# Optimization experiments

Hardware: AMD Instinct MI355X
Metric: run time of the kernel (lower is better)

The kernel has to match this reference:

```python
import jax, jax.numpy as jnp
import numpy as np
import math

NUM_HEADS = 8


def _dwconv(x, w, b, pad):
    # depthwise conv: x (B,C,H,W), w (C,1,k,k)
    c = x.shape[1]
    y = jax.lax.conv_general_dilated(
        x, w, window_strides=(1, 1), padding=[(pad, pad), (pad, pad)],
        feature_group_count=c, dimension_numbers=("NCHW", "OIHW", "NCHW"))
    return y + b[None, :, None, None]


def _conv(x, w, b, pad):
    y = jax.lax.conv_general_dilated(
        x, w, window_strides=(1, 1), padding=[(pad, pad), (pad, pad)],
        dimension_numbers=("NCHW", "OIHW", "NCHW"))
    return y + b[None, :, None, None]


def setup_inputs() -> dict:
    key = jax.random.key(0)
    ks = jax.random.split(key, 6)
    B, C, H, W = 8, 128, 128, 128
    x = jax.random.normal(ks[0], (B, C, H, W), dtype=jnp.float32)
    wq = jax.random.normal(ks[1], (C, 1, 9, 9), dtype=jnp.float32) * 0.05
    wk = jax.random.normal(ks[2], (C, 1, 9, 9), dtype=jnp.float32) * 0.05
    wv = jax.random.normal(ks[3], (C, 1, 9, 9), dtype=jnp.float32) * 0.05
    wo = jax.random.normal(ks[4], (C, C, 3, 3), dtype=jnp.float32) * 0.02
    bq = jnp.zeros((C,), jnp.float32)
    bk = jnp.zeros((C,), jnp.float32)
    bv = jnp.zeros((C,), jnp.float32)
    bo = jnp.zeros((C,), jnp.float32)
    return {"x": x, "wq": wq, "bq": bq, "wk": wk, "bk": bk,
            "wv": wv, "bv": bv, "wo": wo, "bo": bo}


def reference(x, wq, bq, wk, bk, wv, bv, wo, bo):
    b, c, h, w = x.shape
    hds = NUM_HEADS
    d = (h * w) // hds  # spatial dim split across heads
    q = _dwconv(x, wq, bq, 4).reshape(b, c, hds, d).transpose(0, 2, 1, 3)  # (b,hds,c,d)
    k = _dwconv(x, wk, bk, 4).reshape(b, c, hds, d).transpose(0, 2, 3, 1)  # (b,hds,d,c)
    v = _dwconv(x, wv, bv, 4).reshape(b, c, hds, d).transpose(0, 2, 1, 3)  # (b,hds,c,d)
    # channel attention: C x C scores per head, fp32 softmax
    qk = jnp.einsum("bhcd,bhde->bhce", q.astype(jnp.float32), k.astype(jnp.float32)) / math.sqrt(h * w)
    a = jnp.einsum("bhce,bhed->bhcd", jax.nn.softmax(qk, axis=-1), v.astype(jnp.float32))
    a = a.transpose(0, 2, 1, 3).reshape(b, c, h, w)
    return _conv(a, wo, bo, 1)
```

## Files before the change

### kernel.cpp

```cpp
#include <hip/hip_runtime.h>

#define BATCH 8
#define CH 128
#define HH 128
#define WW 128
#define HWSZ 16384
#define NHEADS 8
#define DHEAD 2048

typedef short bf16x8 __attribute__((ext_vector_type(8)));
typedef short bf16x4v __attribute__((ext_vector_type(4)));
typedef float f32x4 __attribute__((ext_vector_type(4)));
typedef float f32x2 __attribute__((ext_vector_type(2)));
typedef _Float16 f16x8 __attribute__((ext_vector_type(8)));
typedef _Float16 f16x4 __attribute__((ext_vector_type(4)));

static __device__ inline unsigned short f2bf(float f) {
    unsigned u = __builtin_bit_cast(unsigned, f);
    u += 0x7fff + ((u >> 16) & 1);
    return (unsigned short)(u >> 16);
}

__global__ __launch_bounds__(256) void toeplitz_prep_kernel(
    const float* __restrict__ wq, const float* __restrict__ wk,
    const float* __restrict__ wv, _Float16* __restrict__ Tp)
{
    const int g = blockIdx.x * 256 + threadIdx.x;
    const int c    = g / 1728;
    const int rem  = g - c * 1728;
    const int m    = rem >> 6;
    const int lane = rem & 63;
    const int conv = m / 9;
    const int dy   = m - conv * 9;
    const float* w = (conv == 0) ? wq : ((conv == 1) ? wk : wv);
    const int j    = lane & 15;
    const int kb   = (lane >> 4) << 3;
    f16x8 h;
    #pragma unroll
    for (int e = 0; e < 8; ++e) {
        const int d = kb + e - j;
        h[e] = (d >= 0 && d <= 8) ? (_Float16)w[c * 81 + dy * 9 + d]
                                  : (_Float16)0.f;
    }
    *(f16x8*)&Tp[(size_t)g * 8] = h;
}

__global__ __launch_bounds__(256) void dwconv_qkv_mfma_kernel(
    const float* __restrict__ x,
    const float* __restrict__ bq, const float* __restrict__ bk,
    const float* __restrict__ bv,
    const _Float16* __restrict__ Tp,
    unsigned short* __restrict__ Qb, unsigned short* __restrict__ Kb,
    unsigned short* __restrict__ Vb)
{
    const int bc = blockIdx.x;
    const int b  = bc >> 7;
    const int c  = bc & (CH - 1);

    __shared__ _Float16 img[136][144];

    const int tid  = threadIdx.x;
    const int wave = tid >> 6;
    const int lane = tid & 63;
    const int lx   = lane & 15;
    const int qd   = lane >> 4;

    f16x8 Btp[27];
    const _Float16* tp = Tp + (size_t)c * 13824 + (size_t)lane * 8;
    #pragma unroll
    for (int m = 0; m < 27; ++m)
        Btp[m] = *(const f16x8*)(tp + (size_t)m * 512);

    {
        f16x8 z = {0, 0, 0, 0, 0, 0, 0, 0};
        _Float16* flat = &img[0][0];
        for (int i = tid; i < 2448; i += 256)
            *(f16x8*)&flat[i * 8] = z;
    }
    __syncthreads();
    const float* xp = x + (size_t)bc * HWSZ;
    for (int i = tid; i < 4096; i += 256) {
        const float4 v = *(const float4*)&xp[i * 4];
        const int y  = i >> 5;
        const int xc = (i & 31) << 2;
        f16x4 h = {(_Float16)v.x, (_Float16)v.y, (_Float16)v.z, (_Float16)v.w};
        *(f16x4*)&img[y + 4][xc + 4] = h;
    }
    __syncthreads();

    const float bqv = bq[c], bkv = bk[c], bvv = bv[c];

    #pragma unroll 1
    for (int t = 0; t < 8; ++t) {
        const int sg = t * 4 + wave;
        const int yg = sg >> 2;
        const int y0 = yg << 4;
        const int x0 = (sg & 3) << 5;

        f32x4 aq0 = {bqv, bqv, bqv, bqv}, aq1 = aq0;
        f32x4 ak0 = {bkv, bkv, bkv, bkv}, ak1 = ak0;
        f32x4 av0 = {bvv, bvv, bvv, bvv}, av1 = av0;

        const _Float16* rp = &img[y0 + lx][x0 + (qd << 3)];
        #pragma unroll
        for (int dy = 0; dy < 9; ++dy) {
            const f16x8 a0 = *(const f16x8*)rp;
            const f16x8 a1 = *(const f16x8*)(rp + 16);
            rp += 144;
            aq0 = __builtin_amdgcn_mfma_f32_16x16x32_f16(a0, Btp[dy],      aq0, 0, 0, 0);
            aq1 = __builtin_amdgcn_mfma_f32_16x16x32_f16(a1, Btp[dy],      aq1, 0, 0, 0);
            ak0 = __builtin_amdgcn_mfma_f32_16x16x32_f16(a0, Btp[9 + dy],  ak0, 0, 0, 0);
            ak1 = __builtin_amdgcn_mfma_f32_16x16x32_f16(a1, Btp[9 + dy],  ak1, 0, 0, 0);
            av0 = __builtin_amdgcn_mfma_f32_16x16x32_f16(a0, Btp[18 + dy], av0, 0, 0, 0);
            av1 = __builtin_amdgcn_mfma_f32_16x16x32_f16(a1, Btp[18 + dy], av1, 0, 0, 0);
        }

        const size_t base = ((size_t)(b * 8 + yg) * CH + c) * DHEAD
                          + (size_t)(qd << 2) * WW + x0 + lx;
        #pragma unroll
        for (int r = 0; r < 4; ++r) {
            Qb[base + r * WW]      = f2bf(aq0[r]);
            Qb[base + r * WW + 16] = f2bf(aq1[r]);
            Kb[base + r * WW]      = f2bf(ak0[r]);
            Kb[base + r * WW + 16] = f2bf(ak1[r]);
            Vb[base + r * WW]      = f2bf(av0[r]);
            Vb[base + r * WW + 16] = f2bf(av1[r]);
        }
    }
}

__global__ __launch_bounds__(256) void qk_mfma_kernel(
    const unsigned short* __restrict__ Qb, const unsigned short* __restrict__ Kb,
    float* __restrict__ Spart)
{
    const int blk   = blockIdx.x;
    const int split = blk & 7;
    const int bh    = blk >> 3;
    const int t0    = split * 256;

    __shared__ unsigned short Qs[128][72];
    __shared__ unsigned short Ks[128][72];

    const int tid  = threadIdx.x;
    const int wave = tid >> 6;
    const int lane = tid & 63;
    const int lx   = lane & 15;
    const int qd   = lane >> 4;
    const int m0   = (wave & 1) * 64;
    const int n0   = (wave >> 1) * 64;

    f32x4 acc[4][4];
    #pragma unroll
    for (int mi = 0; mi < 4; ++mi)
        #pragma unroll
        for (int ni = 0; ni < 4; ++ni) acc[mi][ni] = (f32x4){0.f, 0.f, 0.f, 0.f};

    const unsigned short* Qp = Qb + (size_t)bh * CH * DHEAD;
    const unsigned short* Kp = Kb + (size_t)bh * CH * DHEAD;

    #pragma unroll 1
    for (int tc = 0; tc < 256; tc += 64) {
        __syncthreads();
        for (int i = tid; i < 1024; i += 256) {
            const int r  = i >> 3;
            const int cl = (i & 7) << 3;
            *(bf16x8*)&Qs[r][cl] = *(const bf16x8*)&Qp[(size_t)r * DHEAD + t0 + tc + cl];
            *(bf16x8*)&Ks[r][cl] = *(const bf16x8*)&Kp[(size_t)r * DHEAD + t0 + tc + cl];
        }
        __syncthreads();
        #pragma unroll
        for (int ki = 0; ki < 2; ++ki) {
            const int kc = ki * 32 + qd * 8;
            bf16x8 a[4], bv[4];
            #pragma unroll
            for (int mi = 0; mi < 4; ++mi)
                a[mi] = *(const bf16x8*)&Qs[m0 + mi * 16 + lx][kc];
            #pragma unroll
            for (int ni = 0; ni < 4; ++ni)
                bv[ni] = *(const bf16x8*)&Ks[n0 + ni * 16 + lx][kc];
            #pragma unroll
            for (int mi = 0; mi < 4; ++mi)
                #pragma unroll
                for (int ni = 0; ni < 4; ++ni)
                    acc[mi][ni] = __builtin_amdgcn_mfma_f32_16x16x32_bf16(
                        a[mi], bv[ni], acc[mi][ni], 0, 0, 0);
        }
    }
    float* Sp = Spart + ((size_t)split * 64 + bh) * (CH * CH);
    #pragma unroll
    for (int mi = 0; mi < 4; ++mi)
        #pragma unroll
        for (int r = 0; r < 4; ++r) {
            const int c = m0 + mi * 16 + qd * 4 + r;
            #pragma unroll
            for (int ni = 0; ni < 4; ++ni)
                Sp[c * CH + n0 + ni * 16 + lx] = acc[mi][ni][r];
        }
}

__global__ __launch_bounds__(256) void softmax_kernel(
    const float* __restrict__ Spart, unsigned short* __restrict__ Pb)
{
    const int row  = blockIdx.x * 4 + (threadIdx.x >> 6);
    const int lane = threadIdx.x & 63;
    float v0 = 0.f, v1 = 0.f;
    #pragma unroll
    for (int s = 0; s < 8; ++s) {
        const float* Sp = Spart + (size_t)s * 64 * CH * CH + (size_t)row * CH;
        v0 += Sp[lane];
        v1 += Sp[lane + 64];
    }
    v0 *= 0.0078125f; v1 *= 0.0078125f;
    float m = fmaxf(v0, v1);
    #pragma unroll
    for (int off = 32; off > 0; off >>= 1) m = fmaxf(m, __shfl_down(m, off));
    m = __shfl(m, 0);
    const float e0 = __expf(v0 - m);
    const float e1 = __expf(v1 - m);
    float s = e0 + e1;
    #pragma unroll
    for (int off = 32; off > 0; off >>= 1) s += __shfl_down(s, off);
    s = __shfl(s, 0);
    const float inv = 1.f / s;
    Pb[(size_t)row * CH + lane]      = f2bf(e0 * inv);
    Pb[(size_t)row * CH + lane + 64] = f2bf(e1 * inv);
}

__global__ __launch_bounds__(256) void pv_mfma_kernel(
    const unsigned short* __restrict__ Pb, const unsigned short* __restrict__ Vb,
    unsigned short* __restrict__ At)
{
    const int blk = blockIdx.x;
    const int t0  = (blk & 15) << 7;
    const int bh  = blk >> 4;

    __shared__ __align__(16) char smem[69632];
    unsigned short (*Ps)[136] = (unsigned short(*)[136])smem;
    unsigned short (*Vs)[136] = (unsigned short(*)[136])(smem + 34816);
    float (*So)[132] = (float(*)[132])smem;

    const int tid  = threadIdx.x;
    const int wave = tid >> 6;
    const int lane = tid & 63;
    const int lx   = lane & 15;
    const int qd   = lane >> 4;
    const int m0   = (wave & 1) * 64;
    const int n0   = (wave >> 1) * 64;

    const unsigned short* Pp = Pb + (size_t)bh * CH * CH;
    const unsigned short* Vp = Vb + (size_t)bh * CH * DHEAD;

    for (int i = tid; i < 2048; i += 256) {
        const int r  = i >> 4;
        const int cl = (i & 15) << 3;
        *(bf16x8*)&Ps[r][cl] = *(const bf16x8*)&Pp[(size_t)r * CH + cl];
    }
    for (int i = tid; i < 2048; i += 256) {
        const int e   = i & 127;
        const int tc8 = (i >> 7) << 3;
        const bf16x8 vv = *(const bf16x8*)&Vp[(size_t)e * DHEAD + t0 + tc8];
        #pragma unroll
        for (int j = 0; j < 8; ++j) Vs[tc8 + j][e] = (unsigned short)vv[j];
    }
    __syncthreads();

    f32x4 acc[4][4];
    #pragma unroll
    for (int mi = 0; mi < 4; ++mi)
        #pragma unroll
        for (int ni = 0; ni < 4; ++ni) acc[mi][ni] = (f32x4){0.f, 0.f, 0.f, 0.f};

    #pragma unroll
    for (int ki = 0; ki < 4; ++ki) {
        const int kc = ki * 32 + qd * 8;
        bf16x8 a[4], bv[4];
        #pragma unroll
        for (int mi = 0; mi < 4; ++mi)
            a[mi] = *(const bf16x8*)&Ps[m0 + mi * 16 + lx][kc];
        #pragma unroll
        for (int ni = 0; ni < 4; ++ni)
            bv[ni] = *(const bf16x8*)&Vs[n0 + ni * 16 + lx][kc];
        #pragma unroll
        for (int mi = 0; mi < 4; ++mi)
            #pragma unroll
            for (int ni = 0; ni < 4; ++ni)
                acc[mi][ni] = __builtin_amdgcn_mfma_f32_16x16x32_bf16(
                    a[mi], bv[ni], acc[mi][ni], 0, 0, 0);
    }

    __syncthreads();
    #pragma unroll
    for (int mi = 0; mi < 4; ++mi)
        #pragma unroll
        for (int ni = 0; ni < 4; ++ni)
            #pragma unroll
            for (int r = 0; r < 4; ++r)
                So[n0 + ni * 16 + lx][m0 + mi * 16 + qd * 4 + r] = acc[mi][ni][r];
    __syncthreads();

    const int t  = tid >> 1;
    const int ch = (tid & 1) * 64;
    const size_t orow = (((size_t)(bh >> 3) * HWSZ) + (size_t)(bh & 7) * DHEAD + t0 + t) * CH + ch;
    #pragma unroll
    for (int j = 0; j < 8; ++j) {
        const float4 f0 = *(const float4*)&So[t][ch + j * 8];
        const float4 f1 = *(const float4*)&So[t][ch + j * 8 + 4];
        bf16x8 h;
        h[0] = (short)f2bf(f0.x); h[1] = (short)f2bf(f0.y);
        h[2] = (short)f2bf(f0.z); h[3] = (short)f2bf(f0.w);
        h[4] = (short)f2bf(f1.x); h[5] = (short)f2bf(f1.y);
        h[6] = (short)f2bf(f1.z); h[7] = (short)f2bf(f1.w);
        *(bf16x8*)&At[orow + j * 8] = h;
    }
}

__global__ __launch_bounds__(256) void wprep_kernel(
    const float* __restrict__ wo, unsigned short* __restrict__ Wt)
{
    const int i = blockIdx.x * 256 + threadIdx.x;
    const int tap = i >> 14;
    const int rem = i & 16383;
    const int co  = rem >> 7;
    const int ci  = rem & 127;
    Wt[i] = f2bf(wo[(size_t)(co * CH + ci) * 9 + tap]);
}

__global__ __launch_bounds__(256, 3) void conv3x3_mfma_kernel(
    const unsigned short* __restrict__ At, const unsigned short* __restrict__ Wt,
    const float* __restrict__ bo, float* __restrict__ out)
{
    const int blk = blockIdx.x;
    const int y   = blk & (HH - 1);
    const int b   = blk >> 7;

    __shared__ unsigned short sA[130][136];
    __shared__ unsigned short sW[128][72];

    const int tid  = threadIdx.x;
    const int wave = tid >> 6;
    const int lane = tid & 63;
    const int lx   = lane & 15;
    const int qd   = lane >> 4;
    const int m0   = (wave & 1) * 64;
    const int n0   = (wave >> 1) * 64;

    for (int i = tid; i < 272; i += 256) {
        const int r   = (i < 136) ? 0 : 129;
        const int col = (i < 136) ? i : (i - 136);
        sA[r][col] = 0;
    }

    f32x4 acc[4][4];
    #pragma unroll
    for (int mi = 0; mi < 4; ++mi) {
        f32x4 bv;
        #pragma unroll
        for (int r = 0; r < 4; ++r) bv[r] = bo[m0 + mi * 16 + qd * 4 + r];
        #pragma unroll
        for (int ni = 0; ni < 4; ++ni) acc[mi][ni] = bv;
    }

    const size_t abase = (size_t)b * HWSZ * CH;

    for (int dy = 0; dy < 3; ++dy) {
        const int gy = y + dy - 1;
        __syncthreads();
        if ((unsigned)gy < HH) {
            const unsigned short* row = At + abase + (size_t)gy * WW * CH;
            for (int i = tid; i < 2048; i += 256) {
                const int xx  = i >> 4;
                const int cc8 = (i & 15) << 3;
                *(float4*)&sA[xx + 1][cc8] = *(const float4*)&row[xx * CH + cc8];
            }
        } else {
            const float4 z = make_float4(0.f, 0.f, 0.f, 0.f);
            for (int i = tid; i < 2048; i += 256) {
                const int xx  = i >> 4;
                const int cc8 = (i & 15) << 3;
                *(float4*)&sA[xx + 1][cc8] = z;
            }
        }
        for (int dx = 0; dx < 3; ++dx) {
            const int tap = dy * 3 + dx;
            #pragma unroll 1
            for (int kh = 0; kh < 2; ++kh) {
                if (dx | kh) __syncthreads();
                const unsigned short* wt = Wt + (size_t)tap * CH * CH + kh * 64;
                for (int i = tid; i < 1024; i += 256) {
                    const int co  = i >> 3;
                    const int cc8 = (i & 7) << 3;
                    *(float4*)&sW[co][cc8] = *(const float4*)&wt[co * CH + cc8];
                }
                __syncthreads();
                #pragma unroll
                for (int ks = 0; ks < 2; ++ks) {
                    const int kc  = ks * 32 + qd * 8;
                    const int kca = kh * 64 + kc;
                    bf16x8 a[4], bfr[4];
                    #pragma unroll
                    for (int mi = 0; mi < 4; ++mi)
                        a[mi] = *(const bf16x8*)&sW[m0 + mi * 16 + lx][kc];
                    #pragma unroll
                    for (int ni = 0; ni < 4; ++ni)
                        bfr[ni] = *(const bf16x8*)&sA[n0 + ni * 16 + lx + dx][kca];
                    #pragma unroll
                    for (int mi = 0; mi < 4; ++mi)
                        #pragma unroll
                        for (int ni = 0; ni < 4; ++ni)
                            acc[mi][ni] = __builtin_amdgcn_mfma_f32_16x16x32_bf16(
                                a[mi], bfr[ni], acc[mi][ni], 0, 0, 0);
                }
            }
        }
    }

    const size_t obase = (size_t)b * CH * HWSZ + (size_t)y * WW;
    #pragma unroll
    for (int mi = 0; mi < 4; ++mi) {
        #pragma unroll
        for (int r = 0; r < 4; ++r) {
            const int co = m0 + mi * 16 + qd * 4 + r;
            float* orow = out + obase + (size_t)co * HWSZ;
            #pragma unroll
            for (int ni = 0; ni < 4; ++ni)
                orow[n0 + ni * 16 + lx] = acc[mi][ni][r];
        }
    }
}

extern "C" void kernel_launch(void* const* d_in, const int* in_sizes, int n_in,
                              void* d_out, int out_size, void* d_ws, size_t ws_size,
                              hipStream_t stream)
{
    const float* x  = (const float*)d_in[0];
    const float* wq = (const float*)d_in[1];
    const float* bq = (const float*)d_in[2];
    const float* wk = (const float*)d_in[3];
    const float* bk = (const float*)d_in[4];
    const float* wv = (const float*)d_in[5];
    const float* bv = (const float*)d_in[6];
    const float* wo = (const float*)d_in[7];
    const float* bo = (const float*)d_in[8];

    char* ws = (char*)d_ws;
    unsigned short* Qb    = (unsigned short*)(ws);
    unsigned short* Kb    = (unsigned short*)(ws + (size_t)33554432);
    unsigned short* Vb    = (unsigned short*)(ws + (size_t)67108864);
    float*          Spart = (float*)        (ws + (size_t)100663296);
    unsigned short* Pb    = (unsigned short*)(ws + (size_t)134217728);
    unsigned short* At    = (unsigned short*)(ws + (size_t)136314880);
    unsigned short* Wt    = (unsigned short*)(ws + (size_t)169869312);
    _Float16*       Tp    = (_Float16*)      (ws + (size_t)100663296);

    toeplitz_prep_kernel<<<864, 256, 0, stream>>>(wq, wk, wv, Tp);
    dwconv_qkv_mfma_kernel<<<BATCH * CH, 256, 0, stream>>>(x, bq, bk, bv, Tp, Qb, Kb, Vb);
    wprep_kernel<<<576, 256, 0, stream>>>(wo, Wt);
    qk_mfma_kernel<<<64 * 8, 256, 0, stream>>>(Qb, Kb, Spart);
    softmax_kernel<<<2048, 256, 0, stream>>>(Spart, Pb);
    pv_mfma_kernel<<<64 * 16, 256, 0, stream>>>(Pb, Vb, At);
    conv3x3_mfma_kernel<<<BATCH * HH, 256, 0, stream>>>(At, Wt, bo, (float*)d_out);
}
```

Before: 291.4 us.

## Restructure 3x3 output conv to compute two rows per block with swizzled LDS

The output 3x3 conv kernel now uses 512-thread blocks that each produce two output rows. It loads all four needed input rows into LDS once, instead of reloading per dy for every single output row. The LDS layout uses an XOR swizzle to avoid bank conflicts, and the next weight slice is prefetched into registers during the MFMA loop, with a block index remap. The goal is less redundant global traffic for activations and weights and fewer stalls on loads. In exchange, the kernel needs about 146KB of LDS, which limits it to one block per CU and lowers occupancy.

```diff
diff --git a/kernel.cpp b/kernel.cpp
--- a/kernel.cpp
+++ b/kernel.cpp
@@ -325,30 +325,62 @@
     Wt[i] = f2bf(wo[(size_t)(co * CH + ci) * 9 + tap]);
 }
 
-__global__ __launch_bounds__(256, 3) void conv3x3_mfma_kernel(
+__global__ __launch_bounds__(512, 2) void conv3x3_mfma_kernel(
     const unsigned short* __restrict__ At, const unsigned short* __restrict__ Wt,
     const float* __restrict__ bo, float* __restrict__ out)
 {
-    const int blk = blockIdx.x;
-    const int y   = blk & (HH - 1);
-    const int b   = blk >> 7;
-
-    __shared__ unsigned short sA[130][136];
-    __shared__ unsigned short sW[128][72];
+    __shared__ __align__(16) char smem[149504];
+
+    const int w    = ((blockIdx.x & 7) << 6) | (blockIdx.x >> 3);
+    const int yp   = w & 63;
+    const int b    = w >> 6;
+    const int y0   = yp << 1;
 
     const int tid  = threadIdx.x;
     const int wave = tid >> 6;
     const int lane = tid & 63;
     const int lx   = lane & 15;
     const int qd   = lane >> 4;
-    const int m0   = (wave & 1) * 64;
-    const int n0   = (wave >> 1) * 64;
-
-    for (int i = tid; i < 272; i += 256) {
-        const int r   = (i < 136) ? 0 : 129;
-        const int col = (i < 136) ? i : (i - 136);
-        sA[r][col] = 0;
-    }
+    const int m0   = (wave & 1) << 6;
+    const int n0   = (wave >> 1) << 6;
+    const int rsel = n0 >> 7;
+    const int xb   = n0 & 64;
+
+    const int j0 = tid, j1 = tid + 512;
+    const int co0 = j0 >> 3, cu0 = j0 & 7;
+    const int co1 = j1 >> 3, cu1 = j1 & 7;
+    const unsigned swo0 = (unsigned)((co0 * 128 + cu0 * 16) ^ ((co0 & 7) << 4)) + 133120u;
+    const unsigned swo1 = (unsigned)((co1 * 128 + cu1 * 16) ^ ((co1 & 7) << 4)) + 133120u;
+
+    float4 nwa = *(const float4*)&Wt[(size_t)co0 * 128 + cu0 * 8];
+    float4 nwb = *(const float4*)&Wt[(size_t)co1 * 128 + cu1 * 8];
+
+    const size_t abase = (size_t)b * HWSZ * CH;
+    if (tid < 128) {
+        const int r  = tid >> 5;
+        const int cu = tid & 31;
+        const int xp = (cu & 16) ? 129 : 0;
+        const int u  = cu & 15;
+        const unsigned off = (unsigned)(r * 33280 + xp * 256 + u * 16) ^ (((unsigned)xp & 7u) << 4);
+        *(float4*)(smem + off) = make_float4(0.f, 0.f, 0.f, 0.f);
+    }
+    for (int i = tid; i < 8192; i += 512) {
+        const int r   = i >> 11;
+        const int rem = i & 2047;
+        const int xx  = rem >> 4;
+        const int u   = rem & 15;
+        const int gy  = y0 - 1 + r;
+        float4 v = make_float4(0.f, 0.f, 0.f, 0.f);
+        if ((unsigned)gy < HH)
+            v = *(const float4*)&At[abase + (size_t)gy * WW * CH + xx * CH + u * 8];
+        const int xp = xx + 1;
+        const unsigned off = (unsigned)(r * 33280 + xp * 256 + u * 16) ^ (((unsigned)xp & 7u) << 4);
+        *(float4*)(smem + off) = v;
+    }
+    *(float4*)(smem + swo0) = nwa;
+    *(float4*)(smem + swo1) = nwb;
+    nwa = *(const float4*)&Wt[(size_t)co0 * 128 + 64 + cu0 * 8];
+    nwb = *(const float4*)&Wt[(size_t)co1 * 128 + 64 + cu1 * 8];
 
     f32x4 acc[4][4];
     #pragma unroll
@@ -360,61 +392,57 @@
         for (int ni = 0; ni < 4; ++ni) acc[mi][ni] = bv;
     }
 
-    const size_t abase = (size_t)b * HWSZ * CH;
-
-    for (int dy = 0; dy < 3; ++dy) {
-        const int gy = y + dy - 1;
+    __syncthreads();
+
+    #pragma unroll 1
+    for (int s = 0; s < 18; ++s) {
+        const int tap = s >> 1;
+        const int dy  = (tap * 11) >> 5;
+        const int txc = tap - dy * 3;
+        const int kh  = s & 1;
+        const int ra  = rsel + dy;
+
+        #pragma unroll
+        for (int ks = 0; ks < 2; ++ks) {
+            const int wkb = ks * 64 + qd * 16;
+            const int akb = kh * 128 + ks * 64 + qd * 16;
+            bf16x8 a[4], bfr[4];
+            #pragma unroll
+            for (int mi = 0; mi < 4; ++mi) {
+                const int co = m0 + mi * 16 + lx;
+                a[mi] = *(const bf16x8*)(smem + 133120u +
+                        (unsigned)((co * 128 + wkb) ^ ((co & 7) << 4)));
+            }
+            #pragma unroll
+            for (int ni = 0; ni < 4; ++ni) {
+                const int xp = xb + ni * 16 + lx + txc;
+                const unsigned off = (unsigned)(ra * 33280 + xp * 256 + akb)
+                                   ^ (((unsigned)xp & 7u) << 4);
+                bfr[ni] = *(const bf16x8*)(smem + off);
+            }
+            #pragma unroll
+            for (int mi = 0; mi < 4; ++mi)
+                #pragma unroll
+                for (int ni = 0; ni < 4; ++ni)
+                    acc[mi][ni] = __builtin_amdgcn_mfma_f32_16x16x32_bf16(
+                        a[mi], bfr[ni], acc[mi][ni], 0, 0, 0);
+        }
         __syncthreads();
-        if ((unsigned)gy < HH) {
-            const unsigned short* row = At + abase + (size_t)gy * WW * CH;
-            for (int i = tid; i < 2048; i += 256) {
-                const int xx  = i >> 4;
-                const int cc8 = (i & 15) << 3;
-                *(float4*)&sA[xx + 1][cc8] = *(const float4*)&row[xx * CH + cc8];
+        if (s < 17) {
+            *(float4*)(smem + swo0) = nwa;
+            *(float4*)(smem + swo1) = nwb;
+            if (s < 16) {
+                const int s2 = s + 2;
+                const size_t gb = (size_t)(s2 >> 1) * 16384 + (s2 & 1) * 64;
+                nwa = *(const float4*)&Wt[gb + co0 * 128 + cu0 * 8];
+                nwb = *(const float4*)&Wt[gb + co1 * 128 + cu1 * 8];
             }
-        } else {
-            const float4 z = make_float4(0.f, 0.f, 0.f, 0.f);
-            for (int i = tid; i < 2048; i += 256) {
-                const int xx  = i >> 4;
-                const int cc8 = (i & 15) << 3;
-                *(float4*)&sA[xx + 1][cc8] = z;
-            }
-        }
-        for (int dx = 0; dx < 3; ++dx) {
-            const int tap = dy * 3 + dx;
-            #pragma unroll 1
-            for (int kh = 0; kh < 2; ++kh) {
-                if (dx | kh) __syncthreads();
-                const unsigned short* wt = Wt + (size_t)tap * CH * CH + kh * 64;
-                for (int i = tid; i < 1024; i += 256) {
-                    const int co  = i >> 3;
-                    const int cc8 = (i & 7) << 3;
-                    *(float4*)&sW[co][cc8] = *(const float4*)&wt[co * CH + cc8];
-                }
-                __syncthreads();
-                #pragma unroll
-                for (int ks = 0; ks < 2; ++ks) {
-                    const int kc  = ks * 32 + qd * 8;
-                    const int kca = kh * 64 + kc;
-                    bf16x8 a[4], bfr[4];
-                    #pragma unroll
-                    for (int mi = 0; mi < 4; ++mi)
-                        a[mi] = *(const bf16x8*)&sW[m0 + mi * 16 + lx][kc];
-                    #pragma unroll
-                    for (int ni = 0; ni < 4; ++ni)
-                        bfr[ni] = *(const bf16x8*)&sA[n0 + ni * 16 + lx + dx][kca];
-                    #pragma unroll
-                    for (int mi = 0; mi < 4; ++mi)
-                        #pragma unroll
-                        for (int ni = 0; ni < 4; ++ni)
-                            acc[mi][ni] = __builtin_amdgcn_mfma_f32_16x16x32_bf16(
-                                a[mi], bfr[ni], acc[mi][ni], 0, 0, 0);
-                }
-            }
-        }
-    }
-
-    const size_t obase = (size_t)b * CH * HWSZ + (size_t)y * WW;
+            __syncthreads();
+        }
+    }
+
+    const int gy = y0 + rsel;
+    const size_t obase = (size_t)b * CH * HWSZ + (size_t)gy * WW + xb;
     #pragma unroll
     for (int mi = 0; mi < 4; ++mi) {
         #pragma unroll
@@ -423,7 +451,7 @@
             float* orow = out + obase + (size_t)co * HWSZ;
             #pragma unroll
             for (int ni = 0; ni < 4; ++ni)
-                orow[n0 + ni * 16 + lx] = acc[mi][ni][r];
+                orow[ni * 16 + lx] = acc[mi][ni][r];
         }
     }
 }
@@ -458,5 +486,5 @@
     qk_mfma_kernel<<<64 * 8, 256, 0, stream>>>(Qb, Kb, Spart);
     softmax_kernel<<<2048, 256, 0, stream>>>(Spart, Pb);
     pv_mfma_kernel<<<64 * 16, 256, 0, stream>>>(Pb, Vb, At);
-    conv3x3_mfma_kernel<<<BATCH * HH, 256, 0, stream>>>(At, Wt, bo, (float*)d_out);
-}
+    conv3x3_mfma_kernel<<<BATCH * 64, 512, 0, stream>>>(At, Wt, bo, (float*)d_out);
+}
```

New measurement: 268.9 us. 1.08x faster.
